# Kernel optimization log

Measured on AMD Instinct MI355X. Metric: run time of the kernel, lower is better.

The kernel has to match this reference:

```python
import jax, jax.numpy as jnp
import numpy as np

B, S, D, H = 2, 2048, 768, 12
DH = D // H  # 64


def setup_inputs() -> dict:
    key = jax.random.key(0)
    ks = jax.random.split(key, 8)
    std = 1.0 / np.sqrt(D)
    return {
        "q": jax.random.normal(ks[0], (B, S, D), dtype=jnp.float32),
        "k": jax.random.normal(ks[1], (B, S, D), dtype=jnp.float32),
        "v": jax.random.normal(ks[2], (B, S, D), dtype=jnp.float32),
        "Wq": jax.random.normal(ks[3], (D, D), dtype=jnp.float32) * std,
        "bq": jnp.zeros((D,), dtype=jnp.float32),
        "Wk": jax.random.normal(ks[4], (D, D), dtype=jnp.float32) * std,
        "bk": jnp.zeros((D,), dtype=jnp.float32),
        "Wv": jax.random.normal(ks[5], (D, D), dtype=jnp.float32) * std,
        "bv": jnp.zeros((D,), dtype=jnp.float32),
        "Wo": jax.random.normal(ks[6], (D, D), dtype=jnp.float32) * std,
        "bo": jnp.zeros((D,), dtype=jnp.float32),
    }


def reference(q, k, v, Wq, bq, Wk, bk, Wv, bv, Wo, bo):
    b, s, d = q.shape
    # linear projections then split heads: [b, s, d] -> [b, h, s, dh]
    def split(x):
        return x.reshape(b, s, H, DH).transpose(0, 2, 1, 3)

    qh = split(q @ Wq + bq)
    kh = split(k @ Wk + bk)
    vh = split(v @ Wv + bv)

    scale = 1.0 / jnp.sqrt(jnp.asarray(DH, dtype=q.dtype))
    # full [b, h, s, s] score matrix (faithful to the original unfused op)
    scores = jnp.einsum("bhqd,bhkd->bhqk", qh, kh) * scale
    # look-ahead mask: 1 above the diagonal, added as mask * -1e9
    look_ahead = jnp.triu(jnp.ones((s, s), dtype=scores.dtype), k=1)
    scores = scores + look_ahead * (-1e9)

    attn = jax.nn.softmax(scores, axis=-1)  # dropout is identity at inference
    ctx = jnp.einsum("bhqk,bhkd->bhqd", attn, vh)
    ctx = ctx.transpose(0, 2, 1, 3).reshape(b, s, d)
    return ctx @ Wo + bo
```

## Files before the change

### kernel.cpp

```cpp
#include <hip/hip_runtime.h>
#include <hip/hip_bf16.h>
#include <stdint.h>

#define Bz 2
#define Sz 2048
#define Dz 768
#define Hz 12
#define DHz 64
#define Mz (Bz*Sz)
#define NQT16 128

typedef __attribute__((ext_vector_type(4))) float f32x4;
typedef __attribute__((ext_vector_type(8))) short bf16x8;
typedef unsigned short u16;
typedef __attribute__((ext_vector_type(8))) unsigned short u16x8;

__device__ __forceinline__ u16 f2bf(float f) {
  union { float f; uint32_t u; } c; c.f = f;
  uint32_t u = c.u;
  return (u16)((u + 0x7fffu + ((u >> 16) & 1u)) >> 16);
}

#define GLL16(gsrc, ldst) \
  __builtin_amdgcn_global_load_lds((const __attribute__((address_space(1))) void*)(gsrc), \
                                   (__attribute__((address_space(3))) void*)(ldst), 16, 0, 0)

__device__ __forceinline__ f32x4 mfma16(bf16x8 a, bf16x8 b, f32x4 c) {
  return __builtin_amdgcn_mfma_f32_16x16x32_bf16(a, b, c, 0, 0, 0);
}

#define CVTB 1536
__global__ __launch_bounds__(256) void prep_kernel(
    const float* __restrict__ qa, const float* __restrict__ ka, const float* __restrict__ va,
    u16* __restrict__ qo, u16* __restrict__ ko, u16* __restrict__ vo,
    const float* __restrict__ W0, const float* __restrict__ W1,
    const float* __restrict__ W2, const float* __restrict__ W3,
    u16* __restrict__ T0, u16* __restrict__ T1,
    u16* __restrict__ T2, u16* __restrict__ T3)
{
  __shared__ float tile[32][33];
  int bid = blockIdx.x;
  if (bid < 3 * CVTB) {
    int z = bid / CVTB;
    int i = (bid % CVTB) * 256 + threadIdx.x;
    const float* src = (z == 0) ? qa : (z == 1) ? ka : va;
    u16* dst = (z == 0) ? qo : (z == 1) ? ko : vo;
    const float4* s4 = (const float4*)src;
    float4 a = s4[(size_t)i * 2];
    float4 b = s4[(size_t)i * 2 + 1];
    u16x8 o;
    o[0] = f2bf(a.x); o[1] = f2bf(a.y); o[2] = f2bf(a.z); o[3] = f2bf(a.w);
    o[4] = f2bf(b.x); o[5] = f2bf(b.y); o[6] = f2bf(b.z); o[7] = f2bf(b.w);
    *(u16x8*)(dst + (size_t)i * 8) = o;
  } else {
    int w = bid - 3 * CVTB;
    int z = w / 576;
    int rem = w - z * 576;
    int by = rem / 24, bxi = rem - by * 24;
    const float* W = (z == 0) ? W0 : (z == 1) ? W1 : (z == 2) ? W2 : W3;
    u16* Wt = (z == 0) ? T0 : (z == 1) ? T1 : (z == 2) ? T2 : T3;
    int bx = bxi * 32, byy = by * 32;
    int tx = threadIdx.x & 31, ty = threadIdx.x >> 5;
#pragma unroll
    for (int i = 0; i < 32; i += 8)
      tile[ty + i][tx] = W[(size_t)(byy + ty + i) * Dz + bx + tx];
    __syncthreads();
#pragma unroll
    for (int i = 0; i < 32; i += 8)
      Wt[(size_t)(bx + ty + i) * Dz + byy + tx] = f2bf(tile[tx][ty + i]);
  }
}

__device__ __forceinline__ void gemm_core(
    const u16* __restrict__ A, const u16* __restrict__ Wt,
    const float* __restrict__ bias, void* __restrict__ out, int mode, float oscale,
    u16 (*As)[128 * 32], u16 (*Bs)[128 * 32])
{
  const int tid = threadIdx.x;
  const int wid = tid >> 6, lane = tid & 63;
  const int wm = wid >> 1, wn = wid & 1;
  const int m0 = blockIdx.x * 128, n0 = blockIdx.y * 128;
  const int fq = lane >> 4, fr = lane & 15;

  int aoff[2];
#pragma unroll
  for (int c = 0; c < 2; ++c) {
    int off  = (wid * 2 + c) * 1024 + lane * 16;
    int row  = off >> 6;
    int colb = (off & 63) ^ (((row >> 1) & 3) << 4);
    aoff[c]  = row * Dz + (colb >> 1);
  }

  int raddr[4], rbaddr[4];
#pragma unroll
  for (int f = 0; f < 4; ++f) {
    int rowA = wm * 64 + f * 16 + fr;
    raddr[f]  = rowA * 64 + ((fq * 16) ^ (((rowA >> 1) & 3) << 4));
    int rowB = wn * 64 + f * 16 + fr;
    rbaddr[f] = rowB * 64 + ((fq * 16) ^ (((rowB >> 1) & 3) << 4));
  }

  f32x4 acc[4][4];
  const f32x4 zero = {0.f, 0.f, 0.f, 0.f};
#pragma unroll
  for (int i = 0; i < 4; ++i)
#pragma unroll
    for (int j = 0; j < 4; ++j) acc[i][j] = zero;

  const u16* Abase = A + (size_t)m0 * Dz;
  const u16* Bbase = Wt + (size_t)n0 * Dz;

  const int NKT = Dz / 32;
#pragma unroll
  for (int c = 0; c < 2; ++c) {
    GLL16(Abase + aoff[c], (char*)As[0] + (wid * 2 + c) * 1024);
    GLL16(Bbase + aoff[c], (char*)Bs[0] + (wid * 2 + c) * 1024);
  }
  int cur = 0;

  for (int kt = 0; kt < NKT; ++kt) {
    int nx = cur + 1; if (nx == 3) nx = 0;
    if (kt + 1 < NKT) {
      int ke = (kt + 1) * 32;
#pragma unroll
      for (int c = 0; c < 2; ++c) {
        GLL16(Abase + ke + aoff[c], (char*)As[nx] + (wid * 2 + c) * 1024);
        GLL16(Bbase + ke + aoff[c], (char*)Bs[nx] + (wid * 2 + c) * 1024);
      }
      asm volatile("s_waitcnt vmcnt(4)" ::: "memory");
    } else {
      asm volatile("s_waitcnt vmcnt(0)" ::: "memory");
    }
    __builtin_amdgcn_s_barrier();
    __builtin_amdgcn_sched_barrier(0);

    bf16x8 af[4], bf[4];
#pragma unroll
    for (int f = 0; f < 4; ++f) {
      af[f] = *(const bf16x8*)((const char*)As[cur] + raddr[f]);
      bf[f] = *(const bf16x8*)((const char*)Bs[cur] + rbaddr[f]);
    }
    __builtin_amdgcn_s_setprio(1);
#pragma unroll
    for (int i = 0; i < 4; ++i)
#pragma unroll
      for (int j = 0; j < 4; ++j)
        acc[i][j] = mfma16(af[i], bf[j], acc[i][j]);
    __builtin_amdgcn_s_setprio(0);
    cur = nx;
  }

  {
    u16* O = (u16*)out;
#pragma unroll
    for (int i = 0; i < 4; ++i) {
      int grow = m0 + wm * 64 + i * 16 + fq * 4;
#pragma unroll
      for (int j = 0; j < 4; ++j) {
        int gcol = n0 + wn * 64 + j * 16 + fr;
        float bv = bias[gcol];
        int h = gcol >> 6, dh = gcol & 63;
#pragma unroll
        for (int r = 0; r < 4; ++r) {
          int t = grow + r;
          int b = t >> 11, s = t & 2047;
          int bh = b * Hz + h;
          u16 val = f2bf((acc[i][j][r] + bv) * oscale);
          size_t idx;
          if (mode == 0) {
            idx = ((((size_t)bh * 128 + (s >> 4)) * 2 + (dh >> 5)) * 64
                   + ((dh >> 3) & 3) * 16 + (s & 15)) * 8 + (dh & 7);
          } else if (mode == 3) {
            idx = (((((size_t)bh * 32 + (s >> 6)) * 4 + ((s >> 4) & 3)) * 2 + (dh >> 5)) * 64
                   + ((dh >> 3) & 3) * 16 + (s & 15)) * 8 + (dh & 7);
          } else {
            idx = (((((size_t)bh * 32 + (s >> 6)) * 4 + (dh >> 4)) * 2 + ((s >> 5) & 1)) * 64
                   + ((s >> 3) & 3) * 16 + (dh & 15)) * 8 + (s & 7);
          }
          O[idx] = val;
        }
      }
    }
  }
}

__device__ __forceinline__ void gemm_out_core64(
    const u16* __restrict__ A, const u16* __restrict__ Wt,
    const float* __restrict__ bias, float* __restrict__ O,
    u16 (*As)[64 * 32], u16 (*Bs)[128 * 32])
{
  const int tid = threadIdx.x;
  const int wid = tid >> 6, lane = tid & 63;
  const int wm = wid >> 1, wn = wid & 1;
  const int m0 = blockIdx.x * 64, n0 = blockIdx.y * 128;
  const int fq = lane >> 4, fr = lane & 15;

  int aoff;
  {
    int off  = tid * 16;
    int row  = off >> 6;
    int colb = (off & 63) ^ (((row >> 1) & 3) << 4);
    aoff = row * Dz + (colb >> 1);
  }
  int boff[2];
#pragma unroll
  for (int c = 0; c < 2; ++c) {
    int off  = tid * 16 + c * 4096;
    int row  = off >> 6;
    int colb = (off & 63) ^ (((row >> 1) & 3) << 4);
    boff[c] = row * Dz + (colb >> 1);
  }

  int raddr[2], rbaddr[4];
#pragma unroll
  for (int f = 0; f < 2; ++f) {
    int rowA = wm * 32 + f * 16 + fr;
    raddr[f] = rowA * 64 + ((fq * 16) ^ (((rowA >> 1) & 3) << 4));
  }
#pragma unroll
  for (int f = 0; f < 4; ++f) {
    int rowB = wn * 64 + f * 16 + fr;
    rbaddr[f] = rowB * 64 + ((fq * 16) ^ (((rowB >> 1) & 3) << 4));
  }

  f32x4 acc[2][4];
  const f32x4 zero = {0.f, 0.f, 0.f, 0.f};
#pragma unroll
  for (int i = 0; i < 2; ++i)
#pragma unroll
    for (int j = 0; j < 4; ++j) acc[i][j] = zero;

  const u16* Abase = A + (size_t)m0 * Dz;
  const u16* Bbase = Wt + (size_t)n0 * Dz;

  const int NKT = Dz / 32;
  GLL16(Abase + aoff, (char*)As[0] + tid * 16);
#pragma unroll
  for (int c = 0; c < 2; ++c)
    GLL16(Bbase + boff[c], (char*)Bs[0] + tid * 16 + c * 4096);
  int cur = 0;

  for (int kt = 0; kt < NKT; ++kt) {
    int nx = cur + 1; if (nx == 3) nx = 0;
    if (kt + 1 < NKT) {
      int ke = (kt + 1) * 32;
      GLL16(Abase + ke + aoff, (char*)As[nx] + tid * 16);
#pragma unroll
      for (int c = 0; c < 2; ++c)
        GLL16(Bbase + ke + boff[c], (char*)Bs[nx] + tid * 16 + c * 4096);
      asm volatile("s_waitcnt vmcnt(3)" ::: "memory");
    } else {
      asm volatile("s_waitcnt vmcnt(0)" ::: "memory");
    }
    __builtin_amdgcn_s_barrier();
    __builtin_amdgcn_sched_barrier(0);

    bf16x8 af[2], bf[4];
#pragma unroll
    for (int f = 0; f < 2; ++f)
      af[f] = *(const bf16x8*)((const char*)As[cur] + raddr[f]);
#pragma unroll
    for (int f = 0; f < 4; ++f)
      bf[f] = *(const bf16x8*)((const char*)Bs[cur] + rbaddr[f]);
    __builtin_amdgcn_s_setprio(1);
#pragma unroll
    for (int i = 0; i < 2; ++i)
#pragma unroll
      for (int j = 0; j < 4; ++j)
        acc[i][j] = mfma16(af[i], bf[j], acc[i][j]);
    __builtin_amdgcn_s_setprio(0);
    cur = nx;
  }

#pragma unroll
  for (int i = 0; i < 2; ++i) {
    int grow = m0 + wm * 32 + i * 16 + fq * 4;
#pragma unroll
    for (int j = 0; j < 4; ++j) {
      int gcol = n0 + wn * 64 + j * 16 + fr;
      float bv = bias[gcol];
#pragma unroll
      for (int r = 0; r < 4; ++r)
        O[(size_t)(grow + r) * Dz + gcol] = acc[i][j][r] + bv;
    }
  }
}

#define QSCALE 0.1803368801111404f

__global__ __launch_bounds__(256, 3) void gemm_qkv(
    const u16* __restrict__ qb, const u16* __restrict__ kb, const u16* __restrict__ vb,
    const u16* __restrict__ Wqt, const u16* __restrict__ Wkt, const u16* __restrict__ Wvt,
    const float* __restrict__ bq, const float* __restrict__ bk, const float* __restrict__ bv,
    u16* __restrict__ Qf, u16* __restrict__ Kf, u16* __restrict__ Vf)
{
  __shared__ u16 As[3][128 * 32];
  __shared__ u16 Bs[3][128 * 32];
  const u16* A; const u16* W; const float* bias; u16* out; int mode; float osc;
  if (blockIdx.z == 0)      { A = qb; W = Wqt; bias = bq; out = Qf; mode = 0; osc = QSCALE; }
  else if (blockIdx.z == 1) { A = kb; W = Wkt; bias = bk; out = Kf; mode = 3; osc = 1.f; }
  else                      { A = vb; W = Wvt; bias = bv; out = Vf; mode = 1; osc = 1.f; }
  gemm_core(A, W, bias, out, mode, osc, As, Bs);
}

__global__ __launch_bounds__(256, 4) void gemm_out_k(
    const u16* __restrict__ ctx, const u16* __restrict__ Wot,
    const float* __restrict__ bo, float* __restrict__ out)
{
  __shared__ u16 As[3][64 * 32];
  __shared__ u16 Bs[3][128 * 32];
  gemm_out_core64(ctx, Wot, bo, out, As, Bs);
}

__global__ __launch_bounds__(128, 2) void attn_kernel(
    const u16* __restrict__ Qf, const u16* __restrict__ Kf,
    const u16* __restrict__ Vf, u16* __restrict__ ctx)
{
  __shared__ u16 Ps[2][16 * 64];
  __shared__ float o1buf[64 * 16];
  __shared__ float ml1[2][16];
  const int tid = threadIdx.x, wid = tid >> 6, lane = tid & 63;
  const int fq = lane >> 4, fr = lane & 15;
  const int bh = blockIdx.x;
  const int qt = (NQT16 - 1) - blockIdx.y;
  const int b = bh / Hz, h = bh % Hz;
  const int qbase = qt * 16;
  const int nkt = (qbase + 79) >> 6;

  const bf16x8* Qf8 = (const bf16x8*)Qf + (size_t)bh * 128 * 2 * 64;
  const bf16x8* Kf8 = (const bf16x8*)Kf + (size_t)bh * 32 * 8 * 64;
  const bf16x8* Vf8 = (const bf16x8*)Vf + (size_t)bh * 32 * 8 * 64;

  bf16x8 aq[2];
#pragma unroll
  for (int kk = 0; kk < 2; ++kk)
    aq[kk] = Qf8[((size_t)qt * 2 + kk) * 64 + lane];

  const f32x4 zero = {0.f, 0.f, 0.f, 0.f};
  f32x4 o[4];
#pragma unroll
  for (int i = 0; i < 4; ++i) o[i] = zero;
  float m_r[4], l_r[4];
#pragma unroll
  for (int r = 0; r < 4; ++r) { m_r[r] = -1e30f; l_r[r] = 0.f; }

  char* Pw = (char*)Ps[wid];

  if (wid < nkt) {
    bf16x8 kfr[4][2], vfr[4][2];
#pragma unroll
    for (int j = 0; j < 4; ++j)
#pragma unroll
      for (int kk = 0; kk < 2; ++kk)
        kfr[j][kk] = Kf8[((size_t)wid * 8 + j * 2 + kk) * 64 + lane];

    for (int kt = wid; kt < nkt; kt += 2) {
#pragma unroll
      for (int fo = 0; fo < 4; ++fo)
#pragma unroll
        for (int kk = 0; kk < 2; ++kk)
          vfr[fo][kk] = Vf8[((size_t)kt * 8 + fo * 2 + kk) * 64 + lane];

      f32x4 s[4];
#pragma unroll
      for (int j = 0; j < 4; ++j) s[j] = zero;
      __builtin_amdgcn_s_setprio(1);
#pragma unroll
      for (int j = 0; j < 4; ++j)
#pragma unroll
        for (int kk = 0; kk < 2; ++kk)
          s[j] = mfma16(aq[kk], kfr[j][kk], s[j]);
      __builtin_amdgcn_s_setprio(0);

      if (kt + 2 < nkt) {
#pragma unroll
        for (int j = 0; j < 4; ++j)
#pragma unroll
          for (int kk = 0; kk < 2; ++kk)
            kfr[j][kk] = Kf8[((size_t)(kt + 2) * 8 + j * 2 + kk) * 64 + lane];
      }

      if (kt == nkt - 1) {
#pragma unroll
        for (int j = 0; j < 4; ++j) {
          int keyg = kt * 64 + j * 16 + fr;
#pragma unroll
          for (int r = 0; r < 4; ++r)
            if (keyg > qbase + fq * 4 + r) s[j][r] = -1e30f;
        }
      }

      float mt[4];
#pragma unroll
      for (int r = 0; r < 4; ++r) mt[r] = s[0][r];
#pragma unroll
      for (int j = 1; j < 4; ++j)
#pragma unroll
        for (int r = 0; r < 4; ++r) mt[r] = fmaxf(mt[r], s[j][r]);

      int nd = 0;
#pragma unroll
      for (int r = 0; r < 4; ++r) nd |= (mt[r] > m_r[r] + 8.f) ? 1 : 0;
      if (__any(nd)) {
#pragma unroll
        for (int msk = 1; msk < 16; msk <<= 1)
#pragma unroll
          for (int r = 0; r < 4; ++r) mt[r] = fmaxf(mt[r], __shfl_xor(mt[r], msk));
#pragma unroll
        for (int r = 0; r < 4; ++r) {
          float mn = fmaxf(m_r[r], mt[r]);
          float alpha = __builtin_amdgcn_exp2f(m_r[r] - mn);
          m_r[r] = mn;
          l_r[r] *= alpha;
#pragma unroll
          for (int i = 0; i < 4; ++i) o[i][r] *= alpha;
        }
      }

#pragma unroll
      for (int j = 0; j < 4; ++j) {
#pragma unroll
        for (int r = 0; r < 4; ++r) {
          float e = __builtin_amdgcn_exp2f(s[j][r] - m_r[r]);
          l_r[r] += e;
          int qr = fq * 4 + r;
          int key2 = (j * 16 + fr) * 2;
          *(u16*)(Pw + qr * 128 + (key2 ^ ((qr & 7) << 4))) = f2bf(e);
        }
      }

      __builtin_amdgcn_s_setprio(1);
#pragma unroll
      for (int kk = 0; kk < 2; ++kk) {
        int cbP = (kk * 64 + fq * 16) ^ ((fr & 7) << 4);
        bf16x8 pa = *(const bf16x8*)(Pw + fr * 128 + cbP);
#pragma unroll
        for (int fo = 0; fo < 4; ++fo)
          o[fo] = mfma16(pa, vfr[fo][kk], o[fo]);
      }
      __builtin_amdgcn_s_setprio(0);
    }
  }

#pragma unroll
  for (int msk = 1; msk < 16; msk <<= 1)
#pragma unroll
    for (int r = 0; r < 4; ++r) l_r[r] += __shfl_xor(l_r[r], msk);

  if (wid == 1) {
#pragma unroll
    for (int fo = 0; fo < 4; ++fo)
#pragma unroll
      for (int r = 0; r < 4; ++r)
        o1buf[lane * 16 + fo * 4 + r] = o[fo][r];
    if (fr == 0) {
#pragma unroll
      for (int r = 0; r < 4; ++r) {
        ml1[0][fq * 4 + r] = m_r[r];
        ml1[1][fq * 4 + r] = l_r[r];
      }
    }
  }
  __syncthreads();

  if (wid == 0) {
    float a0[4], a1[4], li[4];
#pragma unroll
    for (int r = 0; r < 4; ++r) {
      float m1 = ml1[0][fq * 4 + r];
      float l1 = ml1[1][fq * 4 + r];
      float mm = fmaxf(m_r[r], m1);
      a0[r] = __builtin_amdgcn_exp2f(m_r[r] - mm);
      a1[r] = __builtin_amdgcn_exp2f(m1 - mm);
      li[r] = 1.0f / (l_r[r] * a0[r] + l1 * a1[r]);
    }
#pragma unroll
    for (int fo = 0; fo < 4; ++fo) {
      int dh = fo * 16 + fr;
#pragma unroll
      for (int r = 0; r < 4; ++r) {
        float o1 = o1buf[lane * 16 + fo * 4 + r];
        float val = (o[fo][r] * a0[r] + o1 * a1[r]) * li[r];
        int qg = qbase + fq * 4 + r;
        ctx[((size_t)b * Sz + qg) * Dz + h * DHz + dh] = f2bf(val);
      }
    }
  }
}

extern "C" void kernel_launch(void* const* d_in, const int* in_sizes, int n_in,
                              void* d_out, int out_size, void* d_ws, size_t ws_size,
                              hipStream_t stream) {
  const float* q  = (const float*)d_in[0];
  const float* k  = (const float*)d_in[1];
  const float* v  = (const float*)d_in[2];
  const float* Wq = (const float*)d_in[3];
  const float* bq = (const float*)d_in[4];
  const float* Wk = (const float*)d_in[5];
  const float* bk = (const float*)d_in[6];
  const float* Wv = (const float*)d_in[7];
  const float* bv = (const float*)d_in[8];
  const float* Wo = (const float*)d_in[9];
  const float* bo = (const float*)d_in[10];
  float* out = (float*)d_out;

  char* ws = (char*)d_ws;
  size_t off = 0;
  auto alloc = [&](size_t bytes) {
    void* p = ws + off;
    off += (bytes + 255) & ~(size_t)255;
    return p;
  };
  u16* qb  = (u16*)alloc((size_t)Mz * Dz * 2);
  u16* kb  = (u16*)alloc((size_t)Mz * Dz * 2);
  u16* vb  = (u16*)alloc((size_t)Mz * Dz * 2);
  u16* Wqt = (u16*)alloc((size_t)Dz * Dz * 2);
  u16* Wkt = (u16*)alloc((size_t)Dz * Dz * 2);
  u16* Wvt = (u16*)alloc((size_t)Dz * Dz * 2);
  u16* Wot = (u16*)alloc((size_t)Dz * Dz * 2);
  u16* Qf  = (u16*)alloc((size_t)Bz * Hz * Sz * DHz * 2);
  u16* Kf  = (u16*)alloc((size_t)Bz * Hz * Sz * DHz * 2);
  u16* Vf  = (u16*)alloc((size_t)Bz * Hz * Sz * DHz * 2);
  u16* ctx = (u16*)alloc((size_t)Mz * Dz * 2);

  prep_kernel<<<3 * CVTB + 4 * 576, 256, 0, stream>>>(
      q, k, v, qb, kb, vb, Wq, Wk, Wv, Wo, Wqt, Wkt, Wvt, Wot);

  gemm_qkv<<<dim3(Mz / 128, Dz / 128, 3), 256, 0, stream>>>(
      qb, kb, vb, Wqt, Wkt, Wvt, bq, bk, bv, Qf, Kf, Vf);

  attn_kernel<<<dim3(Bz * Hz, NQT16), 128, 0, stream>>>(Qf, Kf, Vf, ctx);

  gemm_out_k<<<dim3(Mz / 64, Dz / 128), 256, 0, stream>>>(ctx, Wot, bo, out);
}
```

Before: 88.80 us.

## Deepen GEMM prefetch to two stages and pack P stores with permuted V layout

The projection GEMMs now prefetch two k-tiles ahead into the three-slot LDS ring, issuing the next load after the barrier, so global latency is hidden over two iterations. The attention softmax converts probabilities in pairs with v_cvt_pk_bf16_f32 and writes four bf16 per lane in one 8-byte LDS store instead of sixteen scalar u16 stores. The key order inside each 64-key tile is permuted consistently in the V layout to match. This trades more in-flight memory and a layout change for fewer LDS stores and conversions; the vmcnt counts are unchanged, which risks wrong waits.

```diff
diff --git a/kernel.cpp b/kernel.cpp
--- a/kernel.cpp
+++ b/kernel.cpp
@@ -19,6 +19,12 @@
   union { float f; uint32_t u; } c; c.f = f;
   uint32_t u = c.u;
   return (u16)((u + 0x7fffu + ((u >> 16) & 1u)) >> 16);
+}
+
+__device__ __forceinline__ uint32_t cvtpk(float a, float b) {
+  uint32_t r;
+  asm volatile("v_cvt_pk_bf16_f32 %0, %1, %2" : "=v"(r) : "v"(a), "v"(b));
+  return r;
 }
 
 #define GLL16(gsrc, ldst) \
@@ -112,21 +118,17 @@
 
   const int NKT = Dz / 32;
 #pragma unroll
-  for (int c = 0; c < 2; ++c) {
-    GLL16(Abase + aoff[c], (char*)As[0] + (wid * 2 + c) * 1024);
-    GLL16(Bbase + aoff[c], (char*)Bs[0] + (wid * 2 + c) * 1024);
+  for (int t = 0; t < 2; ++t) {
+#pragma unroll
+    for (int c = 0; c < 2; ++c) {
+      GLL16(Abase + t * 32 + aoff[c], (char*)As[t] + (wid * 2 + c) * 1024);
+      GLL16(Bbase + t * 32 + aoff[c], (char*)Bs[t] + (wid * 2 + c) * 1024);
+    }
   }
   int cur = 0;
 
   for (int kt = 0; kt < NKT; ++kt) {
-    int nx = cur + 1; if (nx == 3) nx = 0;
     if (kt + 1 < NKT) {
-      int ke = (kt + 1) * 32;
-#pragma unroll
-      for (int c = 0; c < 2; ++c) {
-        GLL16(Abase + ke + aoff[c], (char*)As[nx] + (wid * 2 + c) * 1024);
-        GLL16(Bbase + ke + aoff[c], (char*)Bs[nx] + (wid * 2 + c) * 1024);
-      }
       asm volatile("s_waitcnt vmcnt(4)" ::: "memory");
     } else {
       asm volatile("s_waitcnt vmcnt(0)" ::: "memory");
@@ -134,6 +136,16 @@
     __builtin_amdgcn_s_barrier();
     __builtin_amdgcn_sched_barrier(0);
 
+    if (kt + 2 < NKT) {
+      int nx2 = cur + 2; if (nx2 >= 3) nx2 -= 3;
+      int ke = (kt + 2) * 32;
+#pragma unroll
+      for (int c = 0; c < 2; ++c) {
+        GLL16(Abase + ke + aoff[c], (char*)As[nx2] + (wid * 2 + c) * 1024);
+        GLL16(Bbase + ke + aoff[c], (char*)Bs[nx2] + (wid * 2 + c) * 1024);
+      }
+    }
+
     bf16x8 af[4], bf[4];
 #pragma unroll
     for (int f = 0; f < 4; ++f) {
@@ -147,7 +159,7 @@
       for (int j = 0; j < 4; ++j)
         acc[i][j] = mfma16(af[i], bf[j], acc[i][j]);
     __builtin_amdgcn_s_setprio(0);
-    cur = nx;
+    cur = cur + 1; if (cur == 3) cur = 0;
   }
 
   {
@@ -174,8 +186,10 @@
             idx = (((((size_t)bh * 32 + (s >> 6)) * 4 + ((s >> 4) & 3)) * 2 + (dh >> 5)) * 64
                    + ((dh >> 3) & 3) * 16 + (s & 15)) * 8 + (dh & 7);
           } else {
-            idx = (((((size_t)bh * 32 + (s >> 6)) * 4 + (dh >> 4)) * 2 + ((s >> 5) & 1)) * 64
-                   + ((s >> 3) & 3) * 16 + (dh & 15)) * 8 + (s & 7);
+            int K  = s & 63;
+            int pk = ((K & 15) << 2) | (K >> 4);
+            idx = (((((size_t)bh * 32 + (s >> 6)) * 4 + (dh >> 4)) * 2 + (pk >> 5)) * 64
+                   + ((pk >> 3) & 3) * 16 + (dh & 15)) * 8 + (pk & 7);
           }
           O[idx] = val;
         }
@@ -234,20 +248,17 @@
   const u16* Bbase = Wt + (size_t)n0 * Dz;
 
   const int NKT = Dz / 32;
-  GLL16(Abase + aoff, (char*)As[0] + tid * 16);
-#pragma unroll
-  for (int c = 0; c < 2; ++c)
-    GLL16(Bbase + boff[c], (char*)Bs[0] + tid * 16 + c * 4096);
+#pragma unroll
+  for (int t = 0; t < 2; ++t) {
+    GLL16(Abase + t * 32 + aoff, (char*)As[t] + tid * 16);
+#pragma unroll
+    for (int c = 0; c < 2; ++c)
+      GLL16(Bbase + t * 32 + boff[c], (char*)Bs[t] + tid * 16 + c * 4096);
+  }
   int cur = 0;
 
   for (int kt = 0; kt < NKT; ++kt) {
-    int nx = cur + 1; if (nx == 3) nx = 0;
     if (kt + 1 < NKT) {
-      int ke = (kt + 1) * 32;
-      GLL16(Abase + ke + aoff, (char*)As[nx] + tid * 16);
-#pragma unroll
-      for (int c = 0; c < 2; ++c)
-        GLL16(Bbase + ke + boff[c], (char*)Bs[nx] + tid * 16 + c * 4096);
       asm volatile("s_waitcnt vmcnt(3)" ::: "memory");
     } else {
       asm volatile("s_waitcnt vmcnt(0)" ::: "memory");
@@ -255,6 +266,15 @@
     __builtin_amdgcn_s_barrier();
     __builtin_amdgcn_sched_barrier(0);
 
+    if (kt + 2 < NKT) {
+      int nx2 = cur + 2; if (nx2 >= 3) nx2 -= 3;
+      int ke = (kt + 2) * 32;
+      GLL16(Abase + ke + aoff, (char*)As[nx2] + tid * 16);
+#pragma unroll
+      for (int c = 0; c < 2; ++c)
+        GLL16(Bbase + ke + boff[c], (char*)Bs[nx2] + tid * 16 + c * 4096);
+    }
+
     bf16x8 af[2], bf[4];
 #pragma unroll
     for (int f = 0; f < 2; ++f)
@@ -269,7 +289,7 @@
       for (int j = 0; j < 4; ++j)
         acc[i][j] = mfma16(af[i], bf[j], acc[i][j]);
     __builtin_amdgcn_s_setprio(0);
-    cur = nx;
+    cur = cur + 1; if (cur == 3) cur = 0;
   }
 
 #pragma unroll
@@ -417,16 +437,21 @@
         }
       }
 
-#pragma unroll
-      for (int j = 0; j < 4; ++j) {
+      float ev[4][4];
+#pragma unroll
+      for (int j = 0; j < 4; ++j)
 #pragma unroll
         for (int r = 0; r < 4; ++r) {
-          float e = __builtin_amdgcn_exp2f(s[j][r] - m_r[r]);
-          l_r[r] += e;
-          int qr = fq * 4 + r;
-          int key2 = (j * 16 + fr) * 2;
-          *(u16*)(Pw + qr * 128 + (key2 ^ ((qr & 7) << 4))) = f2bf(e);
+          ev[j][r] = __builtin_amdgcn_exp2f(s[j][r] - m_r[r]);
+          l_r[r] += ev[j][r];
         }
+#pragma unroll
+      for (int r = 0; r < 4; ++r) {
+        uint2 w;
+        w.x = cvtpk(ev[0][r], ev[1][r]);
+        w.y = cvtpk(ev[2][r], ev[3][r]);
+        int qr = fq * 4 + r;
+        *(uint2*)(Pw + qr * 128 + ((fr * 8) ^ ((qr & 7) << 4))) = w;
       }
 
       __builtin_amdgcn_s_setprio(1);
```

Measured after the change: 90.54 us. About the same (+2.0%).
